# Optimization experiments

Measured on AMD Instinct MI355X. Metric: run time of the kernel, lower is better.

Reference implementation:

```python
import jax, jax.numpy as jnp
import numpy as np

N = 30000
F_IN = 500
HID = 16
OUT = 3
E = 960000


def setup_inputs() -> dict:
    key = jax.random.key(0)
    ks = jax.random.split(key, 10)
    x = jax.random.normal(ks[0], (N, F_IN), dtype=jnp.float32)
    edge_index = jax.random.randint(ks[1], (2, E), 0, N, dtype=jnp.int32)
    # CNN params (torch Conv1d: weight [out, in, k], bias [out])
    s1 = 1.0 / np.sqrt(1 * 3)
    s2 = 1.0 / np.sqrt(HID * 3)
    conv1_w = jax.random.uniform(ks[2], (HID, 1, 3), jnp.float32, -s1, s1)
    conv1_b = jax.random.uniform(ks[3], (HID,), jnp.float32, -s1, s1)
    conv2_w = jax.random.uniform(ks[4], (HID, HID, 3), jnp.float32, -s2, s2)
    conv2_b = jax.random.uniform(ks[5], (HID,), jnp.float32, -s2, s2)
    # GCNConv params (glorot weight [in, out], zero bias)
    g1 = np.sqrt(6.0 / (HID + HID))
    g2 = np.sqrt(6.0 / (HID + OUT))
    gcn1_w = jax.random.uniform(ks[6], (HID, HID), jnp.float32, -g1, g1)
    gcn1_b = jnp.zeros((HID,), jnp.float32)
    gcn2_w = jax.random.uniform(ks[7], (HID, OUT), jnp.float32, -g2, g2)
    gcn2_b = jnp.zeros((OUT,), jnp.float32)
    return {"x": x, "conv1_w": conv1_w, "conv1_b": conv1_b,
            "conv2_w": conv2_w, "conv2_b": conv2_b,
            "gcn1_w": gcn1_w, "gcn1_b": gcn1_b,
            "gcn2_w": gcn2_w, "gcn2_b": gcn2_b,
            "edge_index": edge_index}


def _conv1d(x, w, b):
    # x: [N, C_in, L], w: [C_out, C_in, 3], padding=1
    y = jax.lax.conv_general_dilated(
        x, w, window_strides=(1,), padding=[(1, 1)],
        dimension_numbers=("NCH", "OIH", "NCH"))
    return y + b[None, :, None]


def _gcn_conv(x, w, b, src, dst, n):
    # x: [n, d_in] -> [n, d_out]; Kipf normalization with self-loops
    h = x @ w
    loop = jnp.arange(n, dtype=src.dtype)
    s = jnp.concatenate([src, loop])
    d = jnp.concatenate([dst, loop])
    deg = jax.ops.segment_sum(jnp.ones_like(d, dtype=h.dtype), d, num_segments=n)
    dinv = jnp.where(deg > 0, jax.lax.rsqrt(deg), 0.0)
    norm = dinv[s] * dinv[d]                      # [E+n]
    msg = h[s] * norm[:, None]                    # gather + scale
    return jax.ops.segment_sum(msg, d, num_segments=n) + b


def reference(x, conv1_w, conv1_b, conv2_w, conv2_b,
              gcn1_w, gcn1_b, gcn2_w, gcn2_b, edge_index):
    # CNN feature extractor over feature axis
    h = x[:, None, :]                             # [N, 1, F_IN]
    h = jax.nn.relu(_conv1d(h, conv1_w, conv1_b))  # [N, HID, F_IN]
    h = jax.nn.relu(_conv1d(h, conv2_w, conv2_b))  # [N, HID, F_IN]
    h = jnp.max(h, axis=2)                        # global max pool -> [N, HID]
    # GCN
    src, dst = edge_index[0], edge_index[1]
    n = h.shape[0]
    h = jax.nn.relu(_gcn_conv(h, gcn1_w, gcn1_b, src, dst, n))
    h = _gcn_conv(h, gcn2_w, gcn2_b, src, dst, n)  # [N, OUT]
    return jax.nn.log_softmax(h, axis=1)
```

## Files before the change

kernel.cpp:

```cpp
#include <hip/hip_runtime.h>
#include <hip/hip_bf16.h>

#define N_NODES 30000
#define F_INLEN 500
#define HID 16
#define OUTC 3
#define NEDGE 960000
#define YP 16
#define NBIN 938
#define HBLK 128
#define NCONV 1664
#define EPRH (NEDGE / HBLK)
#define ECAP 1536

typedef float  f32x4 __attribute__((ext_vector_type(4)));
typedef float  f32x2 __attribute__((ext_vector_type(2)));
typedef short  s16x8 __attribute__((ext_vector_type(8)));

static __device__ __forceinline__ unsigned short f2bf(float f) {
    unsigned int u = __float_as_uint(f);
    unsigned int r = (u + 0x7fffu + ((u >> 16) & 1u)) >> 16;
    return (unsigned short)r;
}
static __device__ __forceinline__ unsigned int pack_bf16x2(float v0, float v1) {
#if __has_builtin(__builtin_amdgcn_cvt_pk_bf16_f32)
    typedef __bf16 bf16x2_t __attribute__((ext_vector_type(2)));
    union { bf16x2_t v; unsigned int u; } cv;
    cv.v = __builtin_amdgcn_cvt_pk_bf16_f32(v0, v1);
    return cv.u;
#else
    return __builtin_amdgcn_perm(__float_as_uint(v1), __float_as_uint(v0), 0x07060302);
#endif
}

__global__ __launch_bounds__(256) void hist_kernel(
    const float* __restrict__ w2, short* __restrict__ bfragsG,
    const int* __restrict__ dst, int* __restrict__ degi, int* __restrict__ cntbase)
{
    const int tid = threadIdx.x;
    if (blockIdx.x == HBLK) {
        if (tid < 64) {
            const int n16 = tid & 15, q = tid >> 4;
#pragma unroll
            for (int j = 0; j < 8; j++) {
                {
                    const int c = q * 8 + j;
                    const int t = c >> 4, i = c & 15;
                    bfragsG[tid * 16 + j] = (short)f2bf(w2[n16 * 48 + i * 3 + t]);
                }
                {
                    const int c = 32 + q * 8 + j;
                    short v = 0;
                    if (c < 48) { const int t = c >> 4, i = c & 15; v = (short)f2bf(w2[n16 * 48 + i * 3 + t]); }
                    bfragsG[tid * 16 + 8 + j] = v;
                }
            }
        }
        return;
    }
    __shared__ int histH[NBIN];
    for (int i = tid; i < NBIN; i += 256) histH[i] = 0;
    __syncthreads();
    const int e0 = blockIdx.x * EPRH;
    for (int e = e0 + tid; e < e0 + EPRH; e += 256) {
        const int d = dst[e];
        atomicAdd(&histH[d >> 5], 1);
        atomicAdd(&degi[d], 1);
    }
    __syncthreads();
    for (int i = tid; i < NBIN; i += 256) cntbase[blockIdx.x * NBIN + i] = histH[i];
}

__global__ __launch_bounds__(256, 7) void conv_reorder(
    const float* __restrict__ x,
    const float* __restrict__ w1, const float* __restrict__ b1,
    const float* __restrict__ b2, const short* __restrict__ bfragsG,
    const int* __restrict__ src, const int* __restrict__ dst,
    const int* __restrict__ degi, const int* __restrict__ cntbase,
    int* __restrict__ packed, int* __restrict__ binstart,
    float* __restrict__ h0)
{
    __shared__ __align__(16) unsigned short yh[515 * YP];
    __shared__ __align__(16) float xp2[2][500];
    __shared__ float red[64];

    const int tid = threadIdx.x;

    if (blockIdx.x < HBLK) {
        int* scA    = (int*)yh;
        int* scB    = scA + NBIN;
        int* totb   = scB + NBIN;
        int* cursor = totb + NBIN;
        const int blk = blockIdx.x;
        for (int bin = tid; bin < NBIN; bin += 256) {
            int tot = 0, psum = 0;
            for (int k = 0; k < HBLK; k++) {
                const int c = cntbase[k * NBIN + bin];
                tot += c;
                if (k < blk) psum += c;
            }
            scA[bin]    = tot;
            totb[bin]   = tot;
            cursor[bin] = psum;
        }
        __syncthreads();
        int* pA = scA; int* pB = scB;
        for (int off = 1; off < NBIN; off <<= 1) {
            for (int i = tid; i < NBIN; i += 256)
                pB[i] = pA[i] + ((i >= off) ? pA[i - off] : 0);
            __syncthreads();
            int* tp = pA; pA = pB; pB = tp;
        }
        for (int i = tid; i < NBIN; i += 256) {
            const int excl = pA[i] - totb[i];
            cursor[i] += excl;
            if (blk == 0) binstart[i] = excl;
        }
        if (blk == 0 && tid == 0) binstart[NBIN] = NEDGE;
        __syncthreads();
        const int e0 = blk * EPRH;
        for (int e = e0 + tid; e < e0 + EPRH; e += 256) {
            const int d = dst[e];
            const int pos = atomicAdd(&cursor[d >> 5], 1);
            packed[pos] = src[e] | (d << 15);
        }
        return;
    }

    const int cb   = blockIdx.x - HBLK;
    const int base = N_NODES / NCONV;
    const int rem  = N_NODES % NCONV;
    const int n0   = cb * base + (cb < rem ? cb : rem);
    const int ncnt = base + (cb < rem ? 1 : 0);

    const int lane = tid & 63;
    const int wave = tid >> 6;
    const int n16  = lane & 15;
    const int q    = lane >> 4;

    if (tid < 240) {
        int row, col;
        if (tid < 16) { row = 0; col = tid; }
        else { row = 501 + (tid - 16) / 16; col = (tid - 16) & 15; }
        yh[row * YP + col] = 0;
    }
    const s16x8* bfp = (const s16x8*)(bfragsG + lane * 16);
    const s16x8 bh0 = bfp[0], bh1 = bfp[1];

    f32x2 wt0[8], wt1[8], wt2[8], bbv[8];
#pragma unroll
    for (int cp = 0; cp < 8; cp++) {
        const int c0 = 2 * cp, c1 = 2 * cp + 1;
        wt0[cp] = (f32x2){w1[c0 * 3 + 0], w1[c1 * 3 + 0]};
        wt1[cp] = (f32x2){w1[c0 * 3 + 1], w1[c1 * 3 + 1]};
        wt2[cp] = (f32x2){w1[c0 * 3 + 2], w1[c1 * 3 + 2]};
        bbv[cp] = (f32x2){b1[c0], b1[c1]};
    }
    const float b2v = (tid < 16) ? b2[tid] : 0.f;

    if (tid < 125) {
        const float4 v = ((const float4*)(x + (long long)n0 * F_INLEN))[tid];
        *((float4*)&xp2[0][tid * 4]) = v;
    }
    int dgn = degi[n0];
    int cur = 0;

    const unsigned short* ybase = yh + (n16 + (q >> 1)) * YP + (q & 1) * 8
                                     + wave * (8 * 16 * YP);

    for (int i = 0; i < ncnt; ++i) {
        const int n = n0 + i;
        float4 pf;
        const bool hp = (i + 1 < ncnt) && (tid < 125);
        if (hp) pf = ((const float4*)(x + (long long)(n + 1) * F_INLEN))[tid];
        const int dgnext = (i + 1 < ncnt) ? degi[n + 1] : 0;

        __syncthreads();

        const float* xc = xp2[cur];
        for (int p = tid; p < 500; p += 256) {
            const float xm = (p > 0)   ? xc[p - 1] : 0.f;
            const float x0 = xc[p];
            const float xr = (p < 499) ? xc[p + 1] : 0.f;
            const f32x2 xv0 = {xm, xm}, xv1 = {x0, x0}, xv2 = {xr, xr};
            const f32x2 zero = {0.f, 0.f};
            unsigned int hpk[8];
#pragma unroll
            for (int cp = 0; cp < 8; cp++) {
                f32x2 a = __builtin_elementwise_fma(wt0[cp], xv0, bbv[cp]);
                a = __builtin_elementwise_fma(wt1[cp], xv1, a);
                a = __builtin_elementwise_fma(wt2[cp], xv2, a);
                a = __builtin_elementwise_max(a, zero);
                hpk[cp] = pack_bf16x2(a[0], a[1]);
            }
            uint4* d = (uint4*)&yh[(p + 1) * YP];
            d[0] = make_uint4(hpk[0], hpk[1], hpk[2], hpk[3]);
            d[1] = make_uint4(hpk[4], hpk[5], hpk[6], hpk[7]);
        }
        __syncthreads();

        f32x4 mxv = {-3.0e38f, -3.0e38f, -3.0e38f, -3.0e38f};
        f32x4 mxt = {-3.0e38f, -3.0e38f, -3.0e38f, -3.0e38f};
#pragma unroll
        for (int it = 0; it < 8; it++) {
            const s16x8 ah0 = *(const s16x8*)(ybase + it * (16 * YP));
            const s16x8 ah1 = *(const s16x8*)(ybase + it * (16 * YP) + 2 * YP);
            f32x4 acc = {0.f, 0.f, 0.f, 0.f};
            acc = __builtin_amdgcn_mfma_f32_16x16x32_bf16(ah0, bh0, acc, 0, 0, 0);
            acc = __builtin_amdgcn_mfma_f32_16x16x32_bf16(ah1, bh1, acc, 0, 0, 0);
            if (it < 7) mxv = __builtin_elementwise_max(mxv, acc);
            else        mxt = __builtin_elementwise_max(mxt, acc);
        }
        if (wave < 3 || q == 0) mxv = __builtin_elementwise_max(mxv, mxt);
        float m = fmaxf(fmaxf(mxv[0], mxv[1]), fmaxf(mxv[2], mxv[3]));
        m = fmaxf(m, __shfl_xor(m, 16));
        m = fmaxf(m, __shfl_xor(m, 32));
        if (lane < 16) red[wave * 16 + lane] = m;

        if (hp) *((float4*)&xp2[cur ^ 1][tid * 4]) = pf;

        __syncthreads();
        if (tid < 16) {
            const float mm = fmaxf(fmaxf(red[tid], red[16 + tid]),
                                   fmaxf(red[32 + tid], red[48 + tid]));
            const float dv = rsqrtf((float)(dgn + 1));
            h0[n * HID + tid] = fmaxf(mm + b2v, 0.f) * dv;
        }
        dgn = dgnext;
        cur ^= 1;
    }
}

__global__ __launch_bounds__(512) void agg1_kernel(
    const int* __restrict__ binstart, int* __restrict__ packed,
    const float* __restrict__ h0,
    const float* __restrict__ W1, const float* __restrict__ b1g,
    const float* __restrict__ W2, float4* __restrict__ t2p4,
    int* __restrict__ binofs)
{
    __shared__ float w1s[256];
    __shared__ float w2s[48];
    __shared__ float b1s[16];
    __shared__ float accS[32 * 17];
    __shared__ int eL[ECAP];
    __shared__ int srt[ECAP];
    __shared__ int h32[32], ls32[32], lofs32[32];
    const int tid = threadIdx.x;
    const int blk = blockIdx.x;
    if (tid < 256) w1s[tid] = W1[tid];
    if (tid < 48) w2s[tid] = W2[tid];
    if (tid < 16) b1s[tid] = b1g[tid];
    if (tid < 32) h32[tid] = 0;
    const int beg = binstart[blk];
    const int cnt = binstart[blk + 1] - beg;
    __syncthreads();
    for (int j = tid; j < cnt; j += 512) {
        const int p = packed[beg + j];
        eL[j] = p;
        atomicAdd(&h32[(p >> 15) & 31], 1);
    }
    __syncthreads();
    if (tid < 32) {
        const int v = h32[tid];
        int inc = v;
#pragma unroll
        for (int off = 1; off < 32; off <<= 1) {
            const int y = __shfl_up(inc, off);
            if (tid >= off) inc += y;
        }
        ls32[tid] = inc - v;
        lofs32[tid] = inc - v;
    }
    __syncthreads();
    for (int j = tid; j < cnt; j += 512) {
        const int p = eL[j];
        const int pos = atomicAdd(&lofs32[(p >> 15) & 31], 1);
        srt[pos] = p;
    }
    __syncthreads();
    for (int j = tid; j < cnt; j += 512) packed[beg + j] = srt[j];
    if (tid < 32) {
        binofs[blk * 64 + tid]      = ls32[tid];
        binofs[blk * 64 + 32 + tid] = h32[tid];
    }
    const int n = tid >> 4;
    const int eslot = (tid >> 2) & 3;
    const int q = tid & 3;
    const int node = blk * 32 + n;
    const bool valid = node < N_NODES;
    f32x4 acc = {0.f, 0.f, 0.f, 0.f};
    if (valid) {
        const int s0 = ls32[n];
        const int s1 = s0 + h32[n];
        for (int i = s0 + eslot; i < s1; i += 4) {
            const int s = srt[i] & 32767;
            acc += *(const f32x4*)(h0 + s * HID + q * 4);
        }
    }
#pragma unroll
    for (int c = 0; c < 4; c++) {
        acc[c] += __shfl_xor(acc[c], 4);
        acc[c] += __shfl_xor(acc[c], 8);
    }
    if (valid && eslot == 0) {
        acc += *(const f32x4*)(h0 + node * HID + q * 4);
        accS[n * 17 + q * 4 + 0] = acc[0];
        accS[n * 17 + q * 4 + 1] = acc[1];
        accS[n * 17 + q * 4 + 2] = acc[2];
        accS[n * 17 + q * 4 + 3] = acc[3];
    }
    __syncthreads();
    if (tid < 128) {
        const int n2 = tid >> 2;
        const int node2 = blk * 32 + n2;
        if (node2 < N_NODES) {
            const float dv = rsqrtf((float)(h32[n2] + 1));
            const int q2 = tid & 3;
            float y0 = 0.f, y1 = 0.f, y2 = 0.f, y3 = 0.f;
#pragma unroll
            for (int i = 0; i < 16; i++) {
                const float a = accS[n2 * 17 + i];
                y0 = fmaf(a, w1s[i * 16 + q2 * 4 + 0], y0);
                y1 = fmaf(a, w1s[i * 16 + q2 * 4 + 1], y1);
                y2 = fmaf(a, w1s[i * 16 + q2 * 4 + 2], y2);
                y3 = fmaf(a, w1s[i * 16 + q2 * 4 + 3], y3);
            }
            float d0 = 0.f, d1 = 0.f, d2 = 0.f;
            const float yv[4] = {y0, y1, y2, y3};
#pragma unroll
            for (int j = 0; j < 4; j++) {
                const int o = q2 * 4 + j;
                const float h = fmaxf(b1s[o] + dv * yv[j], 0.f);
                d0 = fmaf(h, w2s[o * 3 + 0], d0);
                d1 = fmaf(h, w2s[o * 3 + 1], d1);
                d2 = fmaf(h, w2s[o * 3 + 2], d2);
            }
            d0 += __shfl_xor(d0, 1); d0 += __shfl_xor(d0, 2);
            d1 += __shfl_xor(d1, 1); d1 += __shfl_xor(d1, 2);
            d2 += __shfl_xor(d2, 1); d2 += __shfl_xor(d2, 2);
            if (q2 == 0) t2p4[node2] = make_float4(d0 * dv, d1 * dv, d2 * dv, dv);
        }
    }
}

__global__ __launch_bounds__(512) void agg2_kernel(
    const int* __restrict__ binstart, const int* __restrict__ packed,
    const float4* __restrict__ t2p4, const int* __restrict__ binofs,
    const float* __restrict__ b2g, float* __restrict__ out)
{
    __shared__ int eL[ECAP];
    __shared__ int ofs[64];
    const int tid = threadIdx.x;
    const int blk = blockIdx.x;
    const int beg = binstart[blk];
    const int cnt = binstart[blk + 1] - beg;
    if (tid < 64) ofs[tid] = binofs[blk * 64 + tid];
    for (int j = tid; j < cnt; j += 512) eL[j] = packed[beg + j];
    __syncthreads();
    const int n = tid >> 4;
    const int ln16 = tid & 15;
    const int node = blk * 32 + n;
    float a0 = 0.f, a1 = 0.f, a2 = 0.f;
    if (node < N_NODES) {
        const int s0 = ofs[n];
        const int s1 = s0 + ofs[32 + n];
        for (int i = s0 + ln16; i < s1; i += 16) {
            const int s = eL[i] & 32767;
            const float4 v = t2p4[s];
            a0 += v.x; a1 += v.y; a2 += v.z;
        }
    }
#pragma unroll
    for (int msk = 1; msk < 16; msk <<= 1) {
        a0 += __shfl_xor(a0, msk);
        a1 += __shfl_xor(a1, msk);
        a2 += __shfl_xor(a2, msk);
    }
    if (ln16 == 0 && node < N_NODES) {
        const float4 self = t2p4[node];
        const float dv = self.w;
        const float z0 = b2g[0] + dv * (a0 + self.x);
        const float z1 = b2g[1] + dv * (a1 + self.y);
        const float z2 = b2g[2] + dv * (a2 + self.z);
        const float m = fmaxf(z0, fmaxf(z1, z2));
        const float lg = m + logf(expf(z0 - m) + expf(z1 - m) + expf(z2 - m));
        out[node * 3 + 0] = z0 - lg;
        out[node * 3 + 1] = z1 - lg;
        out[node * 3 + 2] = z2 - lg;
    }
}

extern "C" void kernel_launch(void* const* d_in, const int* in_sizes, int n_in,
                              void* d_out, int out_size, void* d_ws, size_t ws_size,
                              hipStream_t stream)
{
    const float* x   = (const float*)d_in[0];
    const float* w1  = (const float*)d_in[1];
    const float* b1  = (const float*)d_in[2];
    const float* w2  = (const float*)d_in[3];
    const float* b2  = (const float*)d_in[4];
    const float* g1w = (const float*)d_in[5];
    const float* g1b = (const float*)d_in[6];
    const float* g2w = (const float*)d_in[7];
    const float* g2b = (const float*)d_in[8];
    const int*   ei  = (const int*)d_in[9];
    const int* src = ei;
    const int* dst = ei + NEDGE;

    float* ws = (float*)d_ws;
    float*  h0      = ws;
    float4* t2p4    = (float4*)(ws + 480000);
    int*    degi    = (int*)(ws + 600000);
    int*    cntbase = (int*)(ws + 630000);
    int*    binstart= (int*)(ws + 750064);
    int*    packed  = (int*)(ws + 751104);
    int*    binofs  = (int*)(ws + 1711104);
    short*  bfragsG = (short*)(ws + 1771136);
    float*  out     = (float*)d_out;

    hipMemsetAsync(degi, 0, N_NODES * sizeof(int), stream);
    hist_kernel<<<HBLK + 1, 256, 0, stream>>>(w2, bfragsG, dst, degi, cntbase);
    conv_reorder<<<HBLK + NCONV, 256, 0, stream>>>(x, w1, b1, b2, bfragsG,
                                                   src, dst, degi, cntbase,
                                                   packed, binstart, h0);
    agg1_kernel<<<NBIN, 512, 0, stream>>>(binstart, packed, h0,
                                          g1w, g1b, g2w, t2p4, binofs);
    agg2_kernel<<<NBIN, 512, 0, stream>>>(binstart, packed, t2p4, binofs, g2b, out);
}
```

Baseline: 223.7 us.

## Use 32x32x16 MFMA for conv2 and read x rows directly from global

Conv2 now runs as a 32x32x16 bf16 MFMA, with three K-steps per 32-position tile instead of pairs of 16x16x32 MFMAs. The weight fragments are repacked in the prep block into three 512-element slabs to match. The LDS double-buffered prefetch of each x row is removed, and the conv1 stage now loads x neighbours straight from global memory, which cuts LDS use and one barrier per node. In exchange, global loads are no longer overlapped with compute, and the padding rows past the last position have to be masked explicitly in the final tile.

```diff
diff --git a/kernel.cpp b/kernel.cpp
--- a/kernel.cpp
+++ b/kernel.cpp
@@ -13,9 +13,10 @@
 #define EPRH (NEDGE / HBLK)
 #define ECAP 1536
 
-typedef float  f32x4 __attribute__((ext_vector_type(4)));
-typedef float  f32x2 __attribute__((ext_vector_type(2)));
-typedef short  s16x8 __attribute__((ext_vector_type(8)));
+typedef float  f32x4  __attribute__((ext_vector_type(4)));
+typedef float  f32x2  __attribute__((ext_vector_type(2)));
+typedef float  f32x16 __attribute__((ext_vector_type(16)));
+typedef short  s16x8  __attribute__((ext_vector_type(8)));
 
 static __device__ __forceinline__ unsigned short f2bf(float f) {
     unsigned int u = __float_as_uint(f);
@@ -39,21 +40,19 @@
 {
     const int tid = threadIdx.x;
     if (blockIdx.x == HBLK) {
-        if (tid < 64) {
-            const int n16 = tid & 15, q = tid >> 4;
+        if (tid < 192) {
+            const int t = tid >> 6;
+            const int l = tid & 63;
+            const int n = l & 31;
+            const int h = l >> 5;
 #pragma unroll
             for (int j = 0; j < 8; j++) {
-                {
-                    const int c = q * 8 + j;
-                    const int t = c >> 4, i = c & 15;
-                    bfragsG[tid * 16 + j] = (short)f2bf(w2[n16 * 48 + i * 3 + t]);
+                short v = 0;
+                if (n < 16) {
+                    const int kk = h * 8 + j;
+                    v = (short)f2bf(w2[n * 48 + kk * 3 + t]);
                 }
-                {
-                    const int c = 32 + q * 8 + j;
-                    short v = 0;
-                    if (c < 48) { const int t = c >> 4, i = c & 15; v = (short)f2bf(w2[n16 * 48 + i * 3 + t]); }
-                    bfragsG[tid * 16 + 8 + j] = v;
-                }
+                bfragsG[t * 512 + l * 8 + j] = v;
             }
         }
         return;
@@ -81,7 +80,6 @@
     float* __restrict__ h0)
 {
     __shared__ __align__(16) unsigned short yh[515 * YP];
-    __shared__ __align__(16) float xp2[2][500];
     __shared__ float red[64];
 
     const int tid = threadIdx.x;
@@ -135,8 +133,8 @@
 
     const int lane = tid & 63;
     const int wave = tid >> 6;
-    const int n16  = lane & 15;
-    const int q    = lane >> 4;
+    const int m32  = lane & 31;
+    const int hh   = lane >> 5;
 
     if (tid < 240) {
         int row, col;
@@ -144,8 +142,9 @@
         else { row = 501 + (tid - 16) / 16; col = (tid - 16) & 15; }
         yh[row * YP + col] = 0;
     }
-    const s16x8* bfp = (const s16x8*)(bfragsG + lane * 16);
-    const s16x8 bh0 = bfp[0], bh1 = bfp[1];
+    const s16x8 bt0 = *(const s16x8*)(bfragsG + 0 * 512 + lane * 8);
+    const s16x8 bt1 = *(const s16x8*)(bfragsG + 1 * 512 + lane * 8);
+    const s16x8 bt2 = *(const s16x8*)(bfragsG + 2 * 512 + lane * 8);
 
     f32x2 wt0[8], wt1[8], wt2[8], bbv[8];
 #pragma unroll
@@ -158,31 +157,18 @@
     }
     const float b2v = (tid < 16) ? b2[tid] : 0.f;
 
-    if (tid < 125) {
-        const float4 v = ((const float4*)(x + (long long)n0 * F_INLEN))[tid];
-        *((float4*)&xp2[0][tid * 4]) = v;
-    }
-    int dgn = degi[n0];
-    int cur = 0;
-
-    const unsigned short* ybase = yh + (n16 + (q >> 1)) * YP + (q & 1) * 8
-                                     + wave * (8 * 16 * YP);
+    const unsigned short* ybw = yh + (wave * 128 + m32) * YP + hh * 8;
 
     for (int i = 0; i < ncnt; ++i) {
-        const int n = n0 + i;
-        float4 pf;
-        const bool hp = (i + 1 < ncnt) && (tid < 125);
-        if (hp) pf = ((const float4*)(x + (long long)(n + 1) * F_INLEN))[tid];
-        const int dgnext = (i + 1 < ncnt) ? degi[n + 1] : 0;
-
-        __syncthreads();
-
-        const float* xc = xp2[cur];
+        const int n   = n0 + i;
+        const int dgn = degi[n];
+        const float* xr = x + (long long)n * F_INLEN;
+
         for (int p = tid; p < 500; p += 256) {
-            const float xm = (p > 0)   ? xc[p - 1] : 0.f;
-            const float x0 = xc[p];
-            const float xr = (p < 499) ? xc[p + 1] : 0.f;
-            const f32x2 xv0 = {xm, xm}, xv1 = {x0, x0}, xv2 = {xr, xr};
+            const float xm = (p > 0)   ? xr[p - 1] : 0.f;
+            const float x0 = xr[p];
+            const float xq = (p < 499) ? xr[p + 1] : 0.f;
+            const f32x2 xv0 = {xm, xm}, xv1 = {x0, x0}, xv2 = {xq, xq};
             const f32x2 zero = {0.f, 0.f};
             unsigned int hpk[8];
 #pragma unroll
@@ -199,26 +185,37 @@
         }
         __syncthreads();
 
-        f32x4 mxv = {-3.0e38f, -3.0e38f, -3.0e38f, -3.0e38f};
-        f32x4 mxt = {-3.0e38f, -3.0e38f, -3.0e38f, -3.0e38f};
-#pragma unroll
-        for (int it = 0; it < 8; it++) {
-            const s16x8 ah0 = *(const s16x8*)(ybase + it * (16 * YP));
-            const s16x8 ah1 = *(const s16x8*)(ybase + it * (16 * YP) + 2 * YP);
-            f32x4 acc = {0.f, 0.f, 0.f, 0.f};
-            acc = __builtin_amdgcn_mfma_f32_16x16x32_bf16(ah0, bh0, acc, 0, 0, 0);
-            acc = __builtin_amdgcn_mfma_f32_16x16x32_bf16(ah1, bh1, acc, 0, 0, 0);
-            if (it < 7) mxv = __builtin_elementwise_max(mxv, acc);
-            else        mxt = __builtin_elementwise_max(mxt, acc);
-        }
-        if (wave < 3 || q == 0) mxv = __builtin_elementwise_max(mxv, mxt);
-        float m = fmaxf(fmaxf(mxv[0], mxv[1]), fmaxf(mxv[2], mxv[3]));
-        m = fmaxf(m, __shfl_xor(m, 16));
+        f32x16 mx = {-3.0e38f, -3.0e38f, -3.0e38f, -3.0e38f,
+                     -3.0e38f, -3.0e38f, -3.0e38f, -3.0e38f,
+                     -3.0e38f, -3.0e38f, -3.0e38f, -3.0e38f,
+                     -3.0e38f, -3.0e38f, -3.0e38f, -3.0e38f};
+#pragma unroll
+        for (int t4 = 0; t4 < 4; t4++) {
+            const unsigned short* yt = ybw + t4 * (32 * YP);
+            const s16x8 a0 = *(const s16x8*)(yt);
+            const s16x8 a1 = *(const s16x8*)(yt + YP);
+            const s16x8 a2 = *(const s16x8*)(yt + 2 * YP);
+            f32x16 acc = {0.f, 0.f, 0.f, 0.f, 0.f, 0.f, 0.f, 0.f,
+                          0.f, 0.f, 0.f, 0.f, 0.f, 0.f, 0.f, 0.f};
+            acc = __builtin_amdgcn_mfma_f32_32x32x16_bf16(a0, bt0, acc, 0, 0, 0);
+            acc = __builtin_amdgcn_mfma_f32_32x32x16_bf16(a1, bt1, acc, 0, 0, 0);
+            acc = __builtin_amdgcn_mfma_f32_32x32x16_bf16(a2, bt2, acc, 0, 0, 0);
+            if (t4 == 3 && wave == 3) {
+                if (hh == 0) {
+                    acc[12] = acc[13] = acc[14] = acc[15] = -3.0e38f;
+                } else {
+                    acc[8]  = acc[9]  = acc[10] = acc[11] = -3.0e38f;
+                    acc[12] = acc[13] = acc[14] = acc[15] = -3.0e38f;
+                }
+            }
+            mx = __builtin_elementwise_max(mx, acc);
+        }
+        float m = fmaxf(fmaxf(fmaxf(mx[0], mx[1]),  fmaxf(mx[2],  mx[3])),
+                        fmaxf(fmaxf(mx[4], mx[5]),  fmaxf(mx[6],  mx[7])));
+        m = fmaxf(m, fmaxf(fmaxf(fmaxf(mx[8],  mx[9]),  fmaxf(mx[10], mx[11])),
+                           fmaxf(fmaxf(mx[12], mx[13]), fmaxf(mx[14], mx[15]))));
         m = fmaxf(m, __shfl_xor(m, 32));
         if (lane < 16) red[wave * 16 + lane] = m;
-
-        if (hp) *((float4*)&xp2[cur ^ 1][tid * 4]) = pf;
-
         __syncthreads();
         if (tid < 16) {
             const float mm = fmaxf(fmaxf(red[tid], red[16 + tid]),
@@ -226,8 +223,6 @@
             const float dv = rsqrtf((float)(dgn + 1));
             h0[n * HID + tid] = fmaxf(mm + b2v, 0.f) * dv;
         }
-        dgn = dgnext;
-        cur ^= 1;
     }
 }
 
```

Result: slower. 468.9 us (+109.6%).
